# Optimization experiments

Hardware: AMD Instinct MI355X
Metric: run time of the kernel (lower is better)

The kernel has to match this reference:

```python
import jax, jax.numpy as jnp
import numpy as np

P0, P1, P2 = 0, 9, 95          # player, status
P3 = 103                        # player_info end / cards start
P4 = P3 + 13 * 740              # 9723, cards end / potions start
P5 = P4 + 43                    # 9766, relics start
P6 = P5 + 180                   # 9946, monsters start
P7 = P6 + 5 * 101               # 10451


def setup_inputs() -> dict:
    key = jax.random.key(0)
    ks = jax.random.split(key, 8)
    def lin(k, out_f, in_f):
        # torch.nn.Linear default init: U(-1/sqrt(in), 1/sqrt(in)), weight [out, in]
        bound = 1.0 / np.sqrt(in_f)
        return jax.random.uniform(k, (out_f, in_f), jnp.float32, -bound, bound)
    return {
        "battle": jax.random.normal(ks[0], (32768, P7), jnp.float32),
        "W_player": lin(ks[1], 4, 9),
        "W_status": lin(ks[2], 16, 86),
        "W_pinfo": lin(ks[3], 2, 8),
        "W_card": lin(ks[4], 32, 740),
        "W_potions": lin(ks[5], 8, 43),
        "W_relics": lin(ks[6], 16, 180),
        "W_monster": lin(ks[7], 16, 101),
    }


def reference(battle, W_player, W_status, W_pinfo, W_card, W_potions, W_relics, W_monster):
    B = battle.shape[0]
    player = battle[:, P0:P1] @ W_player.T                     # [B, 4]
    status = battle[:, P1:P2] @ W_status.T                     # [B, 16]
    pinfo = battle[:, P2:P3] @ W_pinfo.T                       # [B, 2]
    # 13 card segments share one weight -> single batched GEMM
    cards = battle[:, P3:P4].reshape(B, 13, 740)
    cards = jnp.einsum('bsf,of->bso', cards, W_card).reshape(B, 13 * 32)
    potions = battle[:, P4:P5] @ W_potions.T                   # [B, 8]
    relics = battle[:, P5:P6] @ W_relics.T                     # [B, 16]
    # 5 monster segments share one weight
    monsters = battle[:, P6:P7].reshape(B, 5, 101)
    monsters = jnp.einsum('bsf,of->bso', monsters, W_monster).reshape(B, 5 * 16)
    # concat in the module's ModuleList order
    return jnp.concatenate([player, status, pinfo, cards, potions, relics, monsters], axis=-1)
```

## Files before the change

kernel.cpp:

```cpp
#include <hip/hip_runtime.h>
#include <stdint.h>


typedef __attribute__((ext_vector_type(8))) short short8;
typedef __attribute__((ext_vector_type(4))) float f32x4;

__device__ inline unsigned short f2bf(float f) {
  union { float f; uint32_t u; } v; v.f = f;
  uint32_t r = v.u + 0x7FFFu + ((v.u >> 16) & 1u);
  return (unsigned short)(r >> 16);
}

__device__ inline uint32_t cvt2(float lo, float hi) {
  uint32_t r;
  asm("v_cvt_pk_bf16_f32 %0, %1, %2" : "=v"(r) : "v"(lo), "v"(hi));
  return r;
}

union bfrag { short8 s; uint32_t u[4]; };

__device__ inline short8 mk_frag(f32x4 lo, f32x4 hi) {
  bfrag f;
  f.u[0] = cvt2(lo[0], lo[1]);
  f.u[1] = cvt2(lo[2], lo[3]);
  f.u[2] = cvt2(hi[0], hi[1]);
  f.u[3] = cvt2(hi[2], hi[3]);
  return f.s;
}

__device__ inline void gload_dw(const float* g, float* lds) {
  __builtin_amdgcn_global_load_lds(
      (const __attribute__((address_space(1))) void*)g,
      (__attribute__((address_space(3))) void*)lds, 4, 0, 0);
}

__global__ __launch_bounds__(256) void pack_w(const float* __restrict__ Wc,
                                              uint32_t* __restrict__ wout) {
  int el = blockIdx.x * 256 + threadIdx.x;
  if (el >= 12288) return;
  int d  = el & 3;
  int rl = (el >> 2) & 15;
  int kg = (el >> 6) & 3;
  int wn = (el >> 8) & 1;
  int cs = el >> 9;
  int n  = wn * 16 + rl;
  int k  = cs * 32 + kg * 8 + d * 2;
  float v0 = (k     < 740) ? Wc[n * 740 + k]     : 0.0f;
  float v1 = (k + 1 < 740) ? Wc[n * 740 + k + 1] : 0.0f;
  wout[el] = (uint32_t)f2bf(v0) | ((uint32_t)f2bf(v1) << 16);
}

__global__ __launch_bounds__(256, 2) void seg_gemm(
    const float* __restrict__ battle,
    const float* __restrict__ Wplayer, const float* __restrict__ Wstatus,
    const float* __restrict__ Wpinfo,  const float* __restrict__ Wpotions,
    const float* __restrict__ Wrelics, const float* __restrict__ Wmonster,
    const uint32_t* __restrict__ wpack2,
    float* __restrict__ out, const float* __restrict__ zpage)
{
  __shared__ float shm[19456];
  const int bid  = blockIdx.x;
  const int t    = threadIdx.x;
  const int lane = t & 63;
  const int wv   = t >> 6;
  const int rl   = lane & 15;
  const int kg   = lane >> 4;

  if (bid < 16384) {
    const uint32_t g0 = (uint32_t)(bid * 2) * 10451u + 103u;
    const uint32_t g1 = g0 + 10451u;
    #pragma unroll
    for (int r = 0; r < 38; ++r)
      gload_dw(battle + g0 + (uint32_t)(r * 256 + t), &shm[r * 256 + t]);
    #pragma unroll
    for (int r = 0; r < 38; ++r)
      gload_dw(battle + g1 + (uint32_t)(r * 256 + t), &shm[9728 + r * 256 + t]);
    __syncthreads();

    const int wm = wv >> 1;
    const int wn = wv & 1;
    const float* aspan = &shm[wm * 9728];
    const uint32_t abase = (rl < 13) ? (uint32_t)(rl * 740) : 0u;

    f32x4 acc = {0.f, 0.f, 0.f, 0.f};
    for (int ch = 0; ch < 6; ++ch) {
      #pragma unroll
      for (int s = 0; s < 4; ++s) {
        const float* ap = aspan + abase + (uint32_t)(ch * 128 + s * 32 + kg * 8);
        f32x4 lo = *(const f32x4*)ap;
        f32x4 hi = *(const f32x4*)(ap + 4);
        short8 aa = mk_frag(lo, hi);
        const int cs = ch * 4 + s;
        short8 wf = *(const short8*)(wpack2 + (uint32_t)(cs * 512 + wn * 256 + kg * 64 + rl * 4));
        acc = __builtin_amdgcn_mfma_f32_16x16x32_bf16(aa, wf, acc, 0, 0, 0);
      }
    }

    const uint32_t b = (uint32_t)(bid * 2 + wm);
    #pragma unroll
    for (int q = 0; q < 4; ++q) {
      const int sub = kg * 4 + q;
      if (sub < 13)
        out[b * 542u + 22u + (uint32_t)(sub * 32 + wn * 16 + rl)] = acc[q];
    }
    return;
  }

  const int sb = bid - 16384;
  int bloc, nsub, K, NOUT, soff, ooff;
  const float* wp;
  if (sb < 1280)      { bloc = sb;        nsub = 5; K = 101; NOUT = 16; soff = 9946; ooff = 462; wp = Wmonster; }
  else if (sb < 1536) { bloc = sb - 1280; nsub = 1; K = 180; NOUT = 16; soff = 9766; ooff = 446; wp = Wrelics; }
  else if (sb < 1792) { bloc = sb - 1536; nsub = 1; K = 86;  NOUT = 16; soff = 9;    ooff = 4;   wp = Wstatus; }
  else if (sb < 2048) { bloc = sb - 1792; nsub = 1; K = 43;  NOUT = 8;  soff = 9723; ooff = 438; wp = Wpotions; }
  else if (sb < 2304) { bloc = sb - 2048; nsub = 1; K = 9;   NOUT = 4;  soff = 0;    ooff = 0;   wp = Wplayer; }
  else                { bloc = sb - 2304; nsub = 1; K = 8;   NOUT = 2;  soff = 95;   ooff = 20;  wp = Wpinfo; }

  float* lds_a = shm;
  float* lds_w = shm + 4096;

  const int mb = bloc * 128;
  const int r0 = t >> 5;

  uint32_t rb[16];
  #pragma unroll
  for (int i = 0; i < 16; ++i) {
    uint32_t m   = (uint32_t)(mb + r0 + 8 * i);
    uint32_t b   = m / (uint32_t)nsub;
    uint32_t sub = m - b * (uint32_t)nsub;
    rb[i] = b * 10451u + (uint32_t)soff + sub * (uint32_t)K;
  }

  const int klin = t & 31;
  const int lk   = (((klin >> 2) ^ r0) << 2) | (klin & 3);

  f32x4 acc[2] = {};
  const int nch = (K + 31) >> 5;

  for (int ch = 0; ch < nch; ++ch) {
    const int kk = (ch << 5) + lk;
    #pragma unroll
    for (int i = 0; i < 16; ++i) {
      const float* sp = (kk < K) ? (battle + rb[i] + kk) : zpage;
      gload_dw(sp, &lds_a[i * 256 + t]);
    }
    #pragma unroll
    for (int i = 0; i < 4; ++i) {
      const int col = r0 + 8 * i;
      const float* sp = (col < NOUT && kk < K) ? (wp + col * K + kk) : zpage;
      gload_dw(sp, &lds_w[i * 256 + t]);
    }
    __syncthreads();

    short8 af[2], bfr;
    #pragma unroll
    for (int mf = 0; mf < 2; ++mf) {
      const int rr  = wv * 32 + mf * 16 + rl;
      const int g0i = (2 * kg) ^ (rr & 7);
      const int g1i = (2 * kg + 1) ^ (rr & 7);
      f32x4 lo = *(const f32x4*)&lds_a[rr * 32 + g0i * 4];
      f32x4 hi = *(const f32x4*)&lds_a[rr * 32 + g1i * 4];
      af[mf] = mk_frag(lo, hi);
    }
    {
      const int c   = rl;
      const int g0i = (2 * kg) ^ (c & 7);
      const int g1i = (2 * kg + 1) ^ (c & 7);
      f32x4 lo = *(const f32x4*)&lds_w[c * 32 + g0i * 4];
      f32x4 hi = *(const f32x4*)&lds_w[c * 32 + g1i * 4];
      bfr = mk_frag(lo, hi);
    }
    #pragma unroll
    for (int mf = 0; mf < 2; ++mf)
      acc[mf] = __builtin_amdgcn_mfma_f32_16x16x32_bf16(af[mf], bfr, acc[mf], 0, 0, 0);

    __syncthreads();
  }

  #pragma unroll
  for (int mf = 0; mf < 2; ++mf) {
    #pragma unroll
    for (int q = 0; q < 4; ++q) {
      uint32_t m   = (uint32_t)(mb + wv * 32 + mf * 16 + kg * 4 + q);
      uint32_t b   = m / (uint32_t)nsub;
      uint32_t sub = m - b * (uint32_t)nsub;
      uint32_t ob  = b * 542u + (uint32_t)ooff + sub * (uint32_t)NOUT;
      const int col = rl;
      if (col < NOUT) out[ob + col] = acc[mf][q];
    }
  }
}

extern "C" void kernel_launch(void* const* d_in, const int* in_sizes, int n_in,
                              void* d_out, int out_size, void* d_ws, size_t ws_size,
                              hipStream_t stream) {
  const float* battle   = (const float*)d_in[0];
  const float* Wplayer  = (const float*)d_in[1];
  const float* Wstatus  = (const float*)d_in[2];
  const float* Wpinfo   = (const float*)d_in[3];
  const float* Wcard    = (const float*)d_in[4];
  const float* Wpotions = (const float*)d_in[5];
  const float* Wrelics  = (const float*)d_in[6];
  const float* Wmonster = (const float*)d_in[7];
  float* out = (float*)d_out;

  const float* zpage = (const float*)d_ws;
  uint32_t* wpack2 = (uint32_t*)((char*)d_ws + 256);

  hipMemsetAsync(d_ws, 0, 256, stream);
  hipLaunchKernelGGL(pack_w, dim3(48), dim3(256), 0, stream, Wcard, wpack2);
  hipLaunchKernelGGL(seg_gemm, dim3(18944), dim3(256), 0, stream,
                     battle, Wplayer, Wstatus, Wpinfo, Wpotions, Wrelics,
                     Wmonster, (const uint32_t*)wpack2, out, zpage);
}
```

Measured before the change: 299.9 us.

## Give each wave its own batch rows for the card GEMM, loading in halves

The card-segment path now runs 4096 blocks instead of 16384. Each wave independently handles two batch rows, computing all 32 output columns with two accumulators. Card data is streamed into a per-wave LDS buffer in two K-halves, guarded by a wave-local vmcnt wait rather than a block-wide barrier. Staggered s_sleep delays spread out each wave's start. This aims to cut barrier and block-launch overhead and to let waves overlap their loads, but it serialises each wave's load-then-compute with little in-wave pipelining.

```diff
diff --git a/kernel.cpp b/kernel.cpp
--- a/kernel.cpp
+++ b/kernel.cpp
@@ -58,7 +58,7 @@
     const uint32_t* __restrict__ wpack2,
     float* __restrict__ out, const float* __restrict__ zpage)
 {
-  __shared__ float shm[19456];
+  __shared__ float shm[20480];
   const int bid  = blockIdx.x;
   const int t    = threadIdx.x;
   const int lane = t & 63;
@@ -66,47 +66,59 @@
   const int rl   = lane & 15;
   const int kg   = lane >> 4;
 
-  if (bid < 16384) {
-    const uint32_t g0 = (uint32_t)(bid * 2) * 10451u + 103u;
-    const uint32_t g1 = g0 + 10451u;
-    #pragma unroll
-    for (int r = 0; r < 38; ++r)
-      gload_dw(battle + g0 + (uint32_t)(r * 256 + t), &shm[r * 256 + t]);
-    #pragma unroll
-    for (int r = 0; r < 38; ++r)
-      gload_dw(battle + g1 + (uint32_t)(r * 256 + t), &shm[9728 + r * 256 + t]);
-    __syncthreads();
-
-    const int wm = wv >> 1;
-    const int wn = wv & 1;
-    const float* aspan = &shm[wm * 9728];
-    const uint32_t abase = (rl < 13) ? (uint32_t)(rl * 740) : 0u;
-
-    f32x4 acc = {0.f, 0.f, 0.f, 0.f};
-    for (int ch = 0; ch < 6; ++ch) {
+  if (bid < 4096) {
+    float* wbuf = &shm[wv * 5120];
+    const int gw = ((bid << 2) | wv) & 7;
+    for (int i = 0; i < gw; ++i) __builtin_amdgcn_s_sleep(6);
+
+    #pragma unroll 1
+    for (int rr = 0; rr < 2; ++rr) {
+      const uint32_t brow = (uint32_t)(bid * 8 + wv * 2 + rr);
+      const uint32_t row  = brow * 10451u + 103u;
+
+      f32x4 acc0 = {0.f, 0.f, 0.f, 0.f};
+      f32x4 acc1 = {0.f, 0.f, 0.f, 0.f};
+
+      #pragma unroll 1
+      for (int h = 0; h < 2; ++h) {
+        #pragma unroll
+        for (int s = 0; s < 13; ++s)
+          #pragma unroll
+          for (int j = 0; j < 6; ++j)
+            gload_dw(battle + row + (uint32_t)(s * 740 + h * 384 + j * 64 + lane),
+                     &wbuf[s * 388 + j * 64 + lane]);
+
+        asm volatile("s_waitcnt vmcnt(0)" ::: "memory");
+
+        const uint32_t abase = (rl < 13) ? (uint32_t)(rl * 388) : 0u;
+        #pragma unroll
+        for (int c = 0; c < 12; ++c) {
+          const int cs = h * 12 + c;
+          const float* ap = wbuf + abase + (uint32_t)(c * 32 + kg * 8);
+          f32x4 lo = *(const f32x4*)ap;
+          f32x4 hi = *(const f32x4*)(ap + 4);
+          short8 aa = mk_frag(lo, hi);
+          short8 w0 = *(const short8*)(wpack2 + (uint32_t)(cs * 512 + kg * 64 + rl * 4));
+          short8 w1 = *(const short8*)(wpack2 + (uint32_t)(cs * 512 + 256 + kg * 64 + rl * 4));
+          acc0 = __builtin_amdgcn_mfma_f32_16x16x32_bf16(aa, w0, acc0, 0, 0, 0);
+          acc1 = __builtin_amdgcn_mfma_f32_16x16x32_bf16(aa, w1, acc1, 0, 0, 0);
+        }
+      }
+
+      const uint32_t ob = brow * 542u + 22u;
       #pragma unroll
-      for (int s = 0; s < 4; ++s) {
-        const float* ap = aspan + abase + (uint32_t)(ch * 128 + s * 32 + kg * 8);
-        f32x4 lo = *(const f32x4*)ap;
-        f32x4 hi = *(const f32x4*)(ap + 4);
-        short8 aa = mk_frag(lo, hi);
-        const int cs = ch * 4 + s;
-        short8 wf = *(const short8*)(wpack2 + (uint32_t)(cs * 512 + wn * 256 + kg * 64 + rl * 4));
-        acc = __builtin_amdgcn_mfma_f32_16x16x32_bf16(aa, wf, acc, 0, 0, 0);
+      for (int q = 0; q < 4; ++q) {
+        const int sub = kg * 4 + q;
+        if (sub < 13) {
+          out[ob + (uint32_t)(sub * 32 + rl)]      = acc0[q];
+          out[ob + (uint32_t)(sub * 32 + 16 + rl)] = acc1[q];
+        }
       }
     }
-
-    const uint32_t b = (uint32_t)(bid * 2 + wm);
-    #pragma unroll
-    for (int q = 0; q < 4; ++q) {
-      const int sub = kg * 4 + q;
-      if (sub < 13)
-        out[b * 542u + 22u + (uint32_t)(sub * 32 + wn * 16 + rl)] = acc[q];
-    }
     return;
   }
 
-  const int sb = bid - 16384;
+  const int sb = bid - 4096;
   int bloc, nsub, K, NOUT, soff, ooff;
   const float* wp;
   if (sb < 1280)      { bloc = sb;        nsub = 5; K = 101; NOUT = 16; soff = 9946; ooff = 462; wp = Wmonster; }
@@ -209,7 +221,7 @@
 
   hipMemsetAsync(d_ws, 0, 256, stream);
   hipLaunchKernelGGL(pack_w, dim3(48), dim3(256), 0, stream, Wcard, wpack2);
-  hipLaunchKernelGGL(seg_gemm, dim3(18944), dim3(256), 0, stream,
+  hipLaunchKernelGGL(seg_gemm, dim3(6656), dim3(256), 0, stream,
                      battle, Wplayer, Wstatus, Wpinfo, Wpotions, Wrelics,
                      Wmonster, (const uint32_t*)wpack2, out, zpage);
 }
```

Result: slower. 370.4 us (+23.5%).
